# Performance work log

Hardware: AMD Instinct MI355X
Metric: run time of the kernel (lower is better)

The kernel has to match this reference:

```python
import jax, jax.numpy as jnp
import numpy as np


def _bilinear_sample(v, gx, gy, H_, W_):
    # v: (B, H_, W_, nh, Cv); gx, gy: (B, Lq, nh, P) in [0,1] normalized coords.
    # Matches F.grid_sample(mode='bilinear', padding_mode='zeros', align_corners=False).
    x = gx * W_ - 0.5
    y = gy * H_ - 0.5
    x0 = jnp.floor(x)
    y0 = jnp.floor(y)
    dx = x - x0
    dy = y - y0
    x0i = x0.astype(jnp.int32)
    y0i = y0.astype(jnp.int32)
    nh = v.shape[3]
    hidx = jnp.arange(nh)[None, :, None]  # broadcast over (Lq, nh, P)

    def corner(yi, xi):
        valid = (yi >= 0) & (yi < H_) & (xi >= 0) & (xi < W_)
        yc = jnp.clip(yi, 0, H_ - 1)
        xc = jnp.clip(xi, 0, W_ - 1)
        gather = jax.vmap(lambda vb, yb, xb: vb[yb, xb, hidx])  # -> (B, Lq, nh, P, Cv)
        return gather(v, yc, xc) * valid[..., None].astype(v.dtype)

    v00 = corner(y0i, x0i)
    v01 = corner(y0i, x0i + 1)
    v10 = corner(y0i + 1, x0i)
    v11 = corner(y0i + 1, x0i + 1)
    wx0 = (1.0 - dx)[..., None]
    wx1 = dx[..., None]
    wy0 = (1.0 - dy)[..., None]
    wy1 = dy[..., None]
    return wy0 * (wx0 * v00 + wx1 * v01) + wy1 * (wx0 * v10 + wx1 * v11)


def setup_inputs() -> dict:
    key = jax.random.key(0)
    ks = jax.random.split(key, 10)
    C, NH, NL, NP = 256, 8, 4, 4
    B = 1
    shapes = np.array([[128, 128], [64, 64], [32, 32], [16, 16]], dtype=np.int64)
    L_in = int((shapes[:, 0] * shapes[:, 1]).sum())  # 21760
    Lq = L_in
    lsi = np.concatenate([[0], np.cumsum(shapes[:, 0] * shapes[:, 1])[:-1]]).astype(np.int64)

    # sampling_offsets bias init (grid of directions scaled by point index), per _reset_parameters
    thetas = np.arange(NH, dtype=np.float32) * (2.0 * np.pi / NH)
    grid = np.stack([np.cos(thetas), np.sin(thetas)], -1)
    grid = grid / np.abs(grid).max(-1, keepdims=True)
    grid = np.tile(grid[:, None, None, :], (1, NL, NP, 1))
    grid = grid * (np.arange(NP, dtype=np.float32) + 1.0)[None, None, :, None]
    b_off = jnp.asarray(grid.reshape(-1))

    xav = float(np.sqrt(2.0 / (C + C)))
    return {
        "query": jax.random.normal(ks[0], (B, Lq, C), jnp.float32),
        "reference_points": jax.random.uniform(ks[1], (B, Lq, NL, 2), jnp.float32),
        "input_flatten": jax.random.normal(ks[2], (B, L_in, C), jnp.float32),
        "input_spatial_shapes": jnp.asarray(shapes),
        "input_level_start_index": jnp.asarray(lsi),
        "input_padding_mask": jnp.zeros((B, L_in), jnp.bool_),
        "W_off": 0.01 * jax.random.normal(ks[3], (C, NH * NL * NP * 2), jnp.float32),
        "b_off": b_off,
        "W_attn": 0.01 * jax.random.normal(ks[4], (C, NH * NL * NP), jnp.float32),
        "b_attn": jnp.zeros((NH * NL * NP,), jnp.float32),
        "W_v": xav * jax.random.normal(ks[5], (C, C), jnp.float32),
        "b_v": jnp.zeros((C,), jnp.float32),
        "W_out": xav * jax.random.normal(ks[6], (C, C), jnp.float32),
        "b_out": jnp.zeros((C,), jnp.float32),
    }


def reference(query, reference_points, input_flatten, input_spatial_shapes,
              input_level_start_index, input_padding_mask,
              W_off, b_off, W_attn, b_attn, W_v, b_v, W_out, b_out):
    shapes = np.asarray(input_spatial_shapes)  # static spatial shapes (host constants)
    B, Lq, C = query.shape
    NL = shapes.shape[0]
    NH = 8
    Cv = C // NH
    NP = b_off.shape[0] // (NH * NL * 2)

    value = input_flatten @ W_v + b_v
    value = jnp.where(input_padding_mask[..., None], 0.0, value)
    value = value.reshape(B, -1, NH, Cv)

    off = (query @ W_off + b_off).reshape(B, Lq, NH, NL, NP, 2)
    attn = (query @ W_attn + b_attn).reshape(B, Lq, NH, NL * NP)
    attn = jax.nn.softmax(attn, axis=-1).reshape(B, Lq, NH, NL, NP)

    # normalizer is (W, H) per level
    norm = jnp.stack([jnp.asarray(shapes[:, 1]), jnp.asarray(shapes[:, 0])], -1).astype(query.dtype)
    loc = reference_points[:, :, None, :, None, :] + off / norm[None, None, None, :, None, :]

    out = jnp.zeros((B, Lq, NH, Cv), query.dtype)
    start = 0
    for lvl in range(NL):
        H_, W_ = int(shapes[lvl, 0]), int(shapes[lvl, 1])
        v_l = value[:, start:start + H_ * W_].reshape(B, H_, W_, NH, Cv)
        start += H_ * W_
        g = loc[:, :, :, lvl]  # (B, Lq, NH, NP, 2)
        sampled = _bilinear_sample(v_l, g[..., 0], g[..., 1], H_, W_)  # (B, Lq, NH, NP, Cv)
        out = out + jnp.einsum('blhpc,blhp->blhc', sampled, attn[:, :, :, lvl])

    out = out.reshape(B, Lq, C) @ W_out + b_out
    return out  # dropout is identity in eval mode
```

## Files before the change

kernel.cpp:

```cpp
#include <hip/hip_runtime.h>
#include <hip/hip_bf16.h>
#include <hip/hip_fp16.h>


typedef _Float16 f16;
typedef _Float16 f16x8 __attribute__((ext_vector_type(8)));
typedef _Float16 f16x4 __attribute__((ext_vector_type(4)));
typedef _Float16 f16x2 __attribute__((ext_vector_type(2)));
typedef float    f32x4 __attribute__((ext_vector_type(4)));

__device__ __forceinline__ void g2lds16(const void* gp, void* lp) {
    __builtin_amdgcn_global_load_lds(
        (const __attribute__((address_space(1))) unsigned int*)gp,
        (__attribute__((address_space(3))) unsigned int*)lp, 16, 0, 0);
}

template <bool HALF_OUT, bool MASKED>
__global__ __launch_bounds__(512) void gemm_split_f16(
    const f16* __restrict__ A,
    const f16* __restrict__ Bt,
    const float* __restrict__ bias,
    void* __restrict__ Cout, int M, int N,
    const unsigned char* __restrict__ mask)
{
    __shared__ __align__(16) f16 As[64 * 64];
    __shared__ __align__(16) f16 Bs[128 * 64];

    const int tid  = threadIdx.x;
    const int m0   = blockIdx.y * 64, n0 = blockIdx.x * 128;
    const int lane = tid & 63, wid = tid >> 6;
    const int wm   = (wid >> 2) * 32, wn = (wid & 3) * 32;

    f32x4 acc[2][2] = {};

    const int sr  = tid >> 3;
    const int sch = tid & 7;

    for (int kt = 0; kt < 12; ++kt) {
        const int kA = (kt < 8 ? kt : kt - 8) * 64;
        const int kB = kt * 64;
        {
            const int r = sr;
            const int gc = (sch ^ (r & 7)) << 3;
            g2lds16(A + (size_t)(m0 + r) * 512 + kA + gc, &As[r * 64 + sch * 8]);
        }
#pragma unroll
        for (int p = 0; p < 2; ++p) {
            const int r = p * 64 + sr;
            const int gc = (sch ^ (r & 7)) << 3;
            g2lds16(Bt + (size_t)(n0 + r) * 768 + kB + gc, &Bs[r * 64 + sch * 8]);
        }
        __syncthreads();

#pragma unroll
        for (int kf = 0; kf < 2; ++kf) {
            const int kch = kf * 4 + (lane >> 4);
            f16x8 av[2], bv[2];
#pragma unroll
            for (int mf = 0; mf < 2; ++mf) {
                const int row = wm + mf * 16 + (lane & 15);
                av[mf] = *(const f16x8*)&As[row * 64 + ((kch ^ (row & 7)) << 3)];
            }
#pragma unroll
            for (int nf = 0; nf < 2; ++nf) {
                const int row = wn + nf * 16 + (lane & 15);
                bv[nf] = *(const f16x8*)&Bs[row * 64 + ((kch ^ (row & 7)) << 3)];
            }
#pragma unroll
            for (int mf = 0; mf < 2; ++mf)
#pragma unroll
                for (int nf = 0; nf < 2; ++nf)
                    acc[mf][nf] = __builtin_amdgcn_mfma_f32_16x16x32_f16(
                        av[mf], bv[nf], acc[mf][nf], 0, 0, 0);
        }
        __syncthreads();
    }

#pragma unroll
    for (int mf = 0; mf < 2; ++mf) {
        const int rb = m0 + wm + mf * 16 + ((lane >> 4) << 2);
#pragma unroll
        for (int nf = 0; nf < 2; ++nf) {
            const int col = n0 + wn + nf * 16 + (lane & 15);
            const float bc = bias[col];
#pragma unroll
            for (int j = 0; j < 4; ++j) {
                const int row = rb + j;
                float v = acc[mf][nf][j] + bc;
                if (MASKED) v = mask[row] ? 0.f : v;
                if (HALF_OUT)
                    ((__half*)Cout)[(size_t)row * N + col] = __float2half(v);
                else
                    ((float*)Cout)[(size_t)row * N + col] = v;
            }
        }
    }
}

__global__ __launch_bounds__(256) void convA_kernel(
    const float* __restrict__ in, f16* __restrict__ out, int total4)
{
    const int i = blockIdx.x * 256 + threadIdx.x;
    if (i >= total4) return;
    const int m = i >> 6, k4 = (i & 63) << 2;
    const float4 v = reinterpret_cast<const float4*>(in)[i];
    f16x4 hi, lo;
    hi.x = (f16)v.x; lo.x = (f16)(v.x - (float)hi.x);
    hi.y = (f16)v.y; lo.y = (f16)(v.y - (float)hi.y);
    hi.z = (f16)v.z; lo.z = (f16)(v.z - (float)hi.z);
    hi.w = (f16)v.w; lo.w = (f16)(v.w - (float)hi.w);
    *reinterpret_cast<f16x4*>(&out[(size_t)m * 512 + k4])       = hi;
    *reinterpret_cast<f16x4*>(&out[(size_t)m * 512 + 256 + k4]) = lo;
}

__global__ __launch_bounds__(256) void prep_kernel(
    const float* __restrict__ Wv,   const float* __restrict__ Woff,
    const float* __restrict__ Wattn,const float* __restrict__ Wout,
    const float* __restrict__ boff, const float* __restrict__ battn,
    f16* __restrict__ Btv, f16* __restrict__ Btoa, f16* __restrict__ Btout,
    float* __restrict__ boa)
{
    const int i = blockIdx.x * 256 + threadIdx.x;
    constexpr int S0 = 256 * 768, S1 = 256 * 768, S2 = 128 * 768, S3 = 256 * 768;
    if (i < S0) {
        const int n = i / 768, k = i - n * 768, ks = k & 255;
        const float w = Wv[(size_t)ks * 256 + n];
        const f16 h = (f16)w;
        Btv[i] = (k < 512) ? h : (f16)(w - (float)h);
    } else if (i < S0 + S1) {
        const int j = i - S0;
        const int n = j / 768, k = j - n * 768, ks = k & 255;
        const float w = Woff[(size_t)ks * 256 + n];
        const f16 h = (f16)w;
        Btoa[j] = (k < 512) ? h : (f16)(w - (float)h);
    } else if (i < S0 + S1 + S2) {
        const int j = i - S0 - S1;
        const int n = j / 768, k = j - n * 768, ks = k & 255;
        const float w = Wattn[(size_t)ks * 128 + n];
        const f16 h = (f16)w;
        Btoa[(size_t)(256 + n) * 768 + k] = (k < 512) ? h : (f16)(w - (float)h);
    } else if (i < S0 + S1 + S2 + S3) {
        const int j = i - S0 - S1 - S2;
        const int n = j / 768, k = j - n * 768, ks = k & 255;
        const float w = Wout[(size_t)ks * 256 + n];
        const f16 h = (f16)w;
        Btout[j] = (k < 512) ? h : (f16)(w - (float)h);
    } else if (i < S0 + S1 + S2 + S3 + 384) {
        const int j = i - S0 - S1 - S2 - S3;
        boa[j] = (j < 256) ? boff[j] : battn[j - 256];
    }
}

__global__ __launch_bounds__(256) void msda_sample_v2(
    const __half* __restrict__ value,
    const float* __restrict__ offattn,
    const float* __restrict__ refp,
    f16* __restrict__ preA)
{
    __shared__ float s_off[2][256];
    __shared__ float s_ref[2][8];
    __shared__ __align__(16) float s_w[2][512];
    __shared__ __align__(16) int   s_i[2][512];

    const int q0 = blockIdx.x * 2, tid = threadIdx.x;
#pragma unroll
    for (int j = 0; j < 2; ++j) {
        const int idx = tid + j * 256;
        const int ql = idx >> 8, col = idx & 255;
        s_off[ql][col] = offattn[(size_t)(q0 + ql) * 384 + col];
    }
    if (tid < 16) s_ref[tid >> 3][tid & 7] = refp[(size_t)(q0 + (tid >> 3)) * 8 + (tid & 7)];
    __syncthreads();

    {
        const int ql = tid >> 7, slot = tid & 127;
        const int h = slot >> 4, pp = slot & 15, l = pp >> 2, p = pp & 3;
        float v = offattn[(size_t)(q0 + ql) * 384 + 256 + slot];
        float mx = v;
#pragma unroll
        for (int o = 1; o < 16; o <<= 1) mx = fmaxf(mx, __shfl_xor(mx, o, 16));
        const float e = expf(v - mx);
        float s = e;
#pragma unroll
        for (int o = 1; o < 16; o <<= 1) s += __shfl_xor(s, o, 16);
        const float a = e / s;

        const int HW_[4]  = {128, 64, 32, 16};
        const int LSI_[4] = {0, 16384, 20480, 21504};
        const int   Wi = HW_[l];
        const float Wf = (float)Wi;
        const float rx = s_ref[ql][l * 2 + 0], ry = s_ref[ql][l * 2 + 1];
        const float ox = s_off[ql][h * 32 + l * 8 + p * 2 + 0];
        const float oy = s_off[ql][h * 32 + l * 8 + p * 2 + 1];
        const float x = (rx + ox / Wf) * Wf - 0.5f;
        const float y = (ry + oy / Wf) * Wf - 0.5f;
        const float x0f = floorf(x), y0f = floorf(y);
        const float dx = x - x0f, dy = y - y0f;
        const int x0 = (int)x0f, y0 = (int)y0f;
        const int x1 = x0 + 1, y1 = y0 + 1;
        const float vx0 = (x0 >= 0 && x0 < Wi) ? 1.f : 0.f;
        const float vx1 = (x1 >= 0 && x1 < Wi) ? 1.f : 0.f;
        const float vy0 = (y0 >= 0 && y0 < Wi) ? 1.f : 0.f;
        const float vy1 = (y1 >= 0 && y1 < Wi) ? 1.f : 0.f;
        const int xc0 = min(max(x0, 0), Wi - 1), xc1 = min(max(x1, 0), Wi - 1);
        const int yc0 = min(max(y0, 0), Wi - 1), yc1 = min(max(y1, 0), Wi - 1);
        const int base = LSI_[l];
        const int b4 = slot * 4;
        s_i[ql][b4 + 0] = (base + yc0 * Wi + xc0) * 256;
        s_i[ql][b4 + 1] = (base + yc0 * Wi + xc1) * 256;
        s_i[ql][b4 + 2] = (base + yc1 * Wi + xc0) * 256;
        s_i[ql][b4 + 3] = (base + yc1 * Wi + xc1) * 256;
        s_w[ql][b4 + 0] = a * (1.f - dy) * (1.f - dx) * vy0 * vx0;
        s_w[ql][b4 + 1] = a * (1.f - dy) * dx         * vy0 * vx1;
        s_w[ql][b4 + 2] = a * dy         * (1.f - dx) * vy1 * vx0;
        s_w[ql][b4 + 3] = a * dy         * dx         * vy1 * vx1;
    }
    __syncthreads();

    const int ql = tid >> 7, slot = tid & 127;
    const int h = slot >> 4, cp = slot & 15;
    const __half* __restrict__ vb = value + h * 32 + cp * 2;
    float acc0 = 0.f, acc1 = 0.f;
#pragma unroll
    for (int pp = 0; pp < 16; ++pp) {
        const int b = (h * 16 + pp) * 4;
        const int4   idx = *reinterpret_cast<const int4*>(&s_i[ql][b]);
        const float4 w   = *reinterpret_cast<const float4*>(&s_w[ql][b]);
        const __half2 v0 = *reinterpret_cast<const __half2*>(vb + idx.x);
        const __half2 v1 = *reinterpret_cast<const __half2*>(vb + idx.y);
        const __half2 v2 = *reinterpret_cast<const __half2*>(vb + idx.z);
        const __half2 v3 = *reinterpret_cast<const __half2*>(vb + idx.w);
        acc0 = fmaf(w.x, __half2float(v0.x), acc0);
        acc1 = fmaf(w.x, __half2float(v0.y), acc1);
        acc0 = fmaf(w.y, __half2float(v1.x), acc0);
        acc1 = fmaf(w.y, __half2float(v1.y), acc1);
        acc0 = fmaf(w.z, __half2float(v2.x), acc0);
        acc1 = fmaf(w.z, __half2float(v2.y), acc1);
        acc0 = fmaf(w.w, __half2float(v3.x), acc0);
        acc1 = fmaf(w.w, __half2float(v3.y), acc1);
    }
    const int q = q0 + ql;
    const f16 h0 = (f16)acc0, h1 = (f16)acc1;
    const f16 l0 = (f16)(acc0 - (float)h0), l1 = (f16)(acc1 - (float)h1);
    f16x2 hv; hv.x = h0; hv.y = h1;
    f16x2 lv; lv.x = l0; lv.y = l1;
    *reinterpret_cast<f16x2*>(&preA[(size_t)q * 512 + h * 32 + cp * 2])       = hv;
    *reinterpret_cast<f16x2*>(&preA[(size_t)q * 512 + 256 + h * 32 + cp * 2]) = lv;
}

extern "C" void kernel_launch(void* const* d_in, const int* in_sizes, int n_in,
                              void* d_out, int out_size, void* d_ws, size_t ws_size,
                              hipStream_t stream)
{
    const float*         query  = (const float*)d_in[0];
    const float*         refp   = (const float*)d_in[1];
    const float*         inF    = (const float*)d_in[2];
    const unsigned char* mask   = (const unsigned char*)d_in[5];
    const float*         W_off  = (const float*)d_in[6];
    const float*         b_off  = (const float*)d_in[7];
    const float*         W_attn = (const float*)d_in[8];
    const float*         b_attn = (const float*)d_in[9];
    const float*         W_v    = (const float*)d_in[10];
    const float*         b_v    = (const float*)d_in[11];
    const float*         W_out  = (const float*)d_in[12];
    const float*         b_out  = (const float*)d_in[13];
    float*               out    = (float*)d_out;

    const int M = in_sizes[0] / 256;
    if (M % 128 != 0) return;

    const size_t SZ_A1  = (size_t)M * 512 * sizeof(f16);
    const size_t SZ_VAL = (size_t)M * 256 * sizeof(__half);
    const size_t SZ_OA  = (size_t)M * 384 * sizeof(float);
    const size_t SZ_BTV = 256 * 768 * sizeof(f16);
    const size_t SZ_BTO = 384 * 768 * sizeof(f16);
    char* w = (char*)d_ws;
    f16*    A1     = (f16*)w;                      w += SZ_A1;
    __half* valueH = (__half*)w;                   w += SZ_VAL;
    float*  offattn= (float*)w;                    w += SZ_OA;
    f16*    Btv    = (f16*)w;                      w += SZ_BTV;
    f16*    Btoa   = (f16*)w;                      w += SZ_BTO;
    f16*    Btout  = (f16*)w;                      w += SZ_BTV;
    float*  boa    = (float*)w;                    w += 512 * sizeof(float);
    if ((size_t)(w - (char*)d_ws) > ws_size) return;

    const dim3 blk256(256), blk512(512);
    const int convA_blocks = (M * 64 + 255) / 256;
    const int prep_total = 3 * 256 * 768 + 128 * 768 + 384;

    prep_kernel<<<dim3((prep_total + 255) / 256), blk256, 0, stream>>>(
        W_v, W_off, W_attn, W_out, b_off, b_attn, Btv, Btoa, Btout, boa);

    convA_kernel<<<dim3(convA_blocks), blk256, 0, stream>>>(inF, A1, M * 64);
    gemm_split_f16<true, true><<<dim3(2, M / 64), blk512, 0, stream>>>(
        A1, Btv, b_v, valueH, M, 256, mask);

    convA_kernel<<<dim3(convA_blocks), blk256, 0, stream>>>(query, A1, M * 64);
    gemm_split_f16<false, false><<<dim3(3, M / 64), blk512, 0, stream>>>(
        A1, Btoa, boa, offattn, M, 384, nullptr);

    msda_sample_v2<<<dim3(M / 2), blk256, 0, stream>>>(valueH, offattn, refp, A1);

    gemm_split_f16<false, false><<<dim3(2, M / 64), blk512, 0, stream>>>(
        A1, Btout, b_out, out, M, 256, nullptr);
}
```

Measured before the change: 229.2 us.

## Fuse fp32-to-split-f16 conversion into GEMM and double-buffer LDS tiles

Removes the separate convA kernels. Each GEMM now loads its fp32 A rows into registers once and converts them in-kernel into hi/lo f16 parts. The GEMM LDS tiles are double-buffered so the next B tile is fetched and the next A tile staged while MFMAs run on the current one, which drops one barrier per k-step. The sampling kernel writes fp32 output directly (no split) and pads its shared index/weight arrays to reduce bank conflicts. This cuts two kernel launches and the A1 intermediate round-trip through memory, at the cost of more registers and LDS per GEMM block.

```diff
diff --git a/kernel.cpp b/kernel.cpp
--- a/kernel.cpp
+++ b/kernel.cpp
@@ -5,8 +5,6 @@
 
 typedef _Float16 f16;
 typedef _Float16 f16x8 __attribute__((ext_vector_type(8)));
-typedef _Float16 f16x4 __attribute__((ext_vector_type(4)));
-typedef _Float16 f16x2 __attribute__((ext_vector_type(2)));
 typedef float    f32x4 __attribute__((ext_vector_type(4)));
 
 __device__ __forceinline__ void g2lds16(const void* gp, void* lp) {
@@ -16,64 +14,94 @@
 }
 
 template <bool HALF_OUT, bool MASKED>
-__global__ __launch_bounds__(512) void gemm_split_f16(
-    const f16* __restrict__ A,
+__global__ __launch_bounds__(512) void gemm_f32a(
+    const float* __restrict__ Af,
     const f16* __restrict__ Bt,
     const float* __restrict__ bias,
     void* __restrict__ Cout, int M, int N,
     const unsigned char* __restrict__ mask)
 {
-    __shared__ __align__(16) f16 As[64 * 64];
-    __shared__ __align__(16) f16 Bs[128 * 64];
+    __shared__ __align__(16) f16 As[2][64 * 64];
+    __shared__ __align__(16) f16 Bs[2][128 * 64];
 
     const int tid  = threadIdx.x;
     const int m0   = blockIdx.y * 64, n0 = blockIdx.x * 128;
     const int lane = tid & 63, wid = tid >> 6;
     const int wm   = (wid >> 2) * 32, wn = (wid & 3) * 32;
 
+    const int arow = tid >> 3;
+    const int acb  = tid & 7;
+    float4 ar[4][2];
+#pragma unroll
+    for (int g = 0; g < 4; ++g)
+#pragma unroll
+        for (int h2 = 0; h2 < 2; ++h2)
+            ar[g][h2] = *reinterpret_cast<const float4*>(
+                Af + (size_t)(m0 + arow) * 256 + g * 64 + acb * 8 + h2 * 4);
+
     f32x4 acc[2][2] = {};
 
+    auto stageA = [&](int buf, int kt) {
+        const int  g  = kt < 4 ? kt : (kt < 8 ? kt - 4 : kt - 8);
+        const bool lo = (kt >= 4 && kt < 8);
+        f16x8 v;
+#pragma unroll
+        for (int h2 = 0; h2 < 2; ++h2) {
+            const float4 f = ar[g][h2];
+            const float fv[4] = {f.x, f.y, f.z, f.w};
+#pragma unroll
+            for (int j = 0; j < 4; ++j) {
+                const f16 hi = (f16)fv[j];
+                v[h2 * 4 + j] = lo ? (f16)(fv[j] - (float)hi) : hi;
+            }
+        }
+        const int cc = acb ^ (arow & 7);
+        *reinterpret_cast<f16x8*>(&As[buf][arow * 64 + cc * 8]) = v;
+    };
     const int sr  = tid >> 3;
     const int sch = tid & 7;
-
+    auto stageB = [&](int buf, int kt) {
+#pragma unroll
+        for (int p = 0; p < 2; ++p) {
+            const int r  = p * 64 + sr;
+            const int gc = (sch ^ (r & 7)) << 3;
+            g2lds16(Bt + (size_t)(n0 + r) * 768 + kt * 64 + gc,
+                    &Bs[buf][r * 64 + sch * 8]);
+        }
+    };
+
+    stageB(0, 0);
+    stageA(0, 0);
+
+#pragma unroll
     for (int kt = 0; kt < 12; ++kt) {
-        const int kA = (kt < 8 ? kt : kt - 8) * 64;
-        const int kB = kt * 64;
-        {
-            const int r = sr;
-            const int gc = (sch ^ (r & 7)) << 3;
-            g2lds16(A + (size_t)(m0 + r) * 512 + kA + gc, &As[r * 64 + sch * 8]);
-        }
-#pragma unroll
-        for (int p = 0; p < 2; ++p) {
-            const int r = p * 64 + sr;
-            const int gc = (sch ^ (r & 7)) << 3;
-            g2lds16(Bt + (size_t)(n0 + r) * 768 + kB + gc, &Bs[r * 64 + sch * 8]);
-        }
+        const int cur = kt & 1;
         __syncthreads();
 
+        f16x8 av[2][2], bv[2][2];
 #pragma unroll
         for (int kf = 0; kf < 2; ++kf) {
             const int kch = kf * 4 + (lane >> 4);
-            f16x8 av[2], bv[2];
 #pragma unroll
             for (int mf = 0; mf < 2; ++mf) {
                 const int row = wm + mf * 16 + (lane & 15);
-                av[mf] = *(const f16x8*)&As[row * 64 + ((kch ^ (row & 7)) << 3)];
+                av[kf][mf] = *(const f16x8*)&As[cur][row * 64 + ((kch ^ (row & 7)) << 3)];
             }
 #pragma unroll
             for (int nf = 0; nf < 2; ++nf) {
                 const int row = wn + nf * 16 + (lane & 15);
-                bv[nf] = *(const f16x8*)&Bs[row * 64 + ((kch ^ (row & 7)) << 3)];
+                bv[kf][nf] = *(const f16x8*)&Bs[cur][row * 64 + ((kch ^ (row & 7)) << 3)];
             }
+        }
+        if (kt < 11) { stageB(cur ^ 1, kt + 1); stageA(cur ^ 1, kt + 1); }
+#pragma unroll
+        for (int kf = 0; kf < 2; ++kf)
 #pragma unroll
             for (int mf = 0; mf < 2; ++mf)
 #pragma unroll
                 for (int nf = 0; nf < 2; ++nf)
                     acc[mf][nf] = __builtin_amdgcn_mfma_f32_16x16x32_f16(
-                        av[mf], bv[nf], acc[mf][nf], 0, 0, 0);
-        }
-        __syncthreads();
+                        av[kf][mf], bv[kf][nf], acc[mf][nf], 0, 0, 0);
     }
 
 #pragma unroll
@@ -95,22 +123,6 @@
             }
         }
     }
-}
-
-__global__ __launch_bounds__(256) void convA_kernel(
-    const float* __restrict__ in, f16* __restrict__ out, int total4)
-{
-    const int i = blockIdx.x * 256 + threadIdx.x;
-    if (i >= total4) return;
-    const int m = i >> 6, k4 = (i & 63) << 2;
-    const float4 v = reinterpret_cast<const float4*>(in)[i];
-    f16x4 hi, lo;
-    hi.x = (f16)v.x; lo.x = (f16)(v.x - (float)hi.x);
-    hi.y = (f16)v.y; lo.y = (f16)(v.y - (float)hi.y);
-    hi.z = (f16)v.z; lo.z = (f16)(v.z - (float)hi.z);
-    hi.w = (f16)v.w; lo.w = (f16)(v.w - (float)hi.w);
-    *reinterpret_cast<f16x4*>(&out[(size_t)m * 512 + k4])       = hi;
-    *reinterpret_cast<f16x4*>(&out[(size_t)m * 512 + 256 + k4]) = lo;
 }
 
 __global__ __launch_bounds__(256) void prep_kernel(
@@ -151,16 +163,16 @@
     }
 }
 
-__global__ __launch_bounds__(256) void msda_sample_v2(
+__global__ __launch_bounds__(256) void msda_sample_v3(
     const __half* __restrict__ value,
     const float* __restrict__ offattn,
     const float* __restrict__ refp,
-    f16* __restrict__ preA)
+    float* __restrict__ pre)
 {
     __shared__ float s_off[2][256];
     __shared__ float s_ref[2][8];
-    __shared__ __align__(16) float s_w[2][512];
-    __shared__ __align__(16) int   s_i[2][512];
+    __shared__ __align__(16) float s_w[2][576];
+    __shared__ __align__(16) int   s_i[2][576];
 
     const int q0 = blockIdx.x * 2, tid = threadIdx.x;
 #pragma unroll
@@ -205,31 +217,32 @@
         const int xc0 = min(max(x0, 0), Wi - 1), xc1 = min(max(x1, 0), Wi - 1);
         const int yc0 = min(max(y0, 0), Wi - 1), yc1 = min(max(y1, 0), Wi - 1);
         const int base = LSI_[l];
-        const int b4 = slot * 4;
-        s_i[ql][b4 + 0] = (base + yc0 * Wi + xc0) * 256;
-        s_i[ql][b4 + 1] = (base + yc0 * Wi + xc1) * 256;
-        s_i[ql][b4 + 2] = (base + yc1 * Wi + xc0) * 256;
-        s_i[ql][b4 + 3] = (base + yc1 * Wi + xc1) * 256;
-        s_w[ql][b4 + 0] = a * (1.f - dy) * (1.f - dx) * vy0 * vx0;
-        s_w[ql][b4 + 1] = a * (1.f - dy) * dx         * vy0 * vx1;
-        s_w[ql][b4 + 2] = a * dy         * (1.f - dx) * vy1 * vx0;
-        s_w[ql][b4 + 3] = a * dy         * dx         * vy1 * vx1;
+        const int eI = h * 72 + pp * 4;
+        s_i[ql][eI + 0] = (base + yc0 * Wi + xc0) * 512;
+        s_i[ql][eI + 1] = (base + yc0 * Wi + xc1) * 512;
+        s_i[ql][eI + 2] = (base + yc1 * Wi + xc0) * 512;
+        s_i[ql][eI + 3] = (base + yc1 * Wi + xc1) * 512;
+        s_w[ql][eI + 0] = a * (1.f - dy) * (1.f - dx) * vy0 * vx0;
+        s_w[ql][eI + 1] = a * (1.f - dy) * dx         * vy0 * vx1;
+        s_w[ql][eI + 2] = a * dy         * (1.f - dx) * vy1 * vx0;
+        s_w[ql][eI + 3] = a * dy         * dx         * vy1 * vx1;
     }
     __syncthreads();
 
     const int ql = tid >> 7, slot = tid & 127;
     const int h = slot >> 4, cp = slot & 15;
-    const __half* __restrict__ vb = value + h * 32 + cp * 2;
+    const int lb = h * 64 + cp * 4;
+    const char* __restrict__ vbase = (const char*)value;
     float acc0 = 0.f, acc1 = 0.f;
 #pragma unroll
     for (int pp = 0; pp < 16; ++pp) {
-        const int b = (h * 16 + pp) * 4;
-        const int4   idx = *reinterpret_cast<const int4*>(&s_i[ql][b]);
-        const float4 w   = *reinterpret_cast<const float4*>(&s_w[ql][b]);
-        const __half2 v0 = *reinterpret_cast<const __half2*>(vb + idx.x);
-        const __half2 v1 = *reinterpret_cast<const __half2*>(vb + idx.y);
-        const __half2 v2 = *reinterpret_cast<const __half2*>(vb + idx.z);
-        const __half2 v3 = *reinterpret_cast<const __half2*>(vb + idx.w);
+        const int eI = h * 72 + pp * 4;
+        const int4   idx = *reinterpret_cast<const int4*>(&s_i[ql][eI]);
+        const float4 w   = *reinterpret_cast<const float4*>(&s_w[ql][eI]);
+        const __half2 v0 = *reinterpret_cast<const __half2*>(vbase + (idx.x + lb));
+        const __half2 v1 = *reinterpret_cast<const __half2*>(vbase + (idx.y + lb));
+        const __half2 v2 = *reinterpret_cast<const __half2*>(vbase + (idx.z + lb));
+        const __half2 v3 = *reinterpret_cast<const __half2*>(vbase + (idx.w + lb));
         acc0 = fmaf(w.x, __half2float(v0.x), acc0);
         acc1 = fmaf(w.x, __half2float(v0.y), acc1);
         acc0 = fmaf(w.y, __half2float(v1.x), acc0);
@@ -239,13 +252,8 @@
         acc0 = fmaf(w.w, __half2float(v3.x), acc0);
         acc1 = fmaf(w.w, __half2float(v3.y), acc1);
     }
-    const int q = q0 + ql;
-    const f16 h0 = (f16)acc0, h1 = (f16)acc1;
-    const f16 l0 = (f16)(acc0 - (float)h0), l1 = (f16)(acc1 - (float)h1);
-    f16x2 hv; hv.x = h0; hv.y = h1;
-    f16x2 lv; lv.x = l0; lv.y = l1;
-    *reinterpret_cast<f16x2*>(&preA[(size_t)q * 512 + h * 32 + cp * 2])       = hv;
-    *reinterpret_cast<f16x2*>(&preA[(size_t)q * 512 + 256 + h * 32 + cp * 2]) = lv;
+    float2 o; o.x = acc0; o.y = acc1;
+    *reinterpret_cast<float2*>(&pre[(size_t)(q0 + ql) * 256 + h * 32 + cp * 2]) = o;
 }
 
 extern "C" void kernel_launch(void* const* d_in, const int* in_sizes, int n_in,
@@ -269,15 +277,15 @@
     const int M = in_sizes[0] / 256;
     if (M % 128 != 0) return;
 
-    const size_t SZ_A1  = (size_t)M * 512 * sizeof(f16);
     const size_t SZ_VAL = (size_t)M * 256 * sizeof(__half);
     const size_t SZ_OA  = (size_t)M * 384 * sizeof(float);
+    const size_t SZ_PRE = (size_t)M * 256 * sizeof(float);
     const size_t SZ_BTV = 256 * 768 * sizeof(f16);
     const size_t SZ_BTO = 384 * 768 * sizeof(f16);
     char* w = (char*)d_ws;
-    f16*    A1     = (f16*)w;                      w += SZ_A1;
     __half* valueH = (__half*)w;                   w += SZ_VAL;
     float*  offattn= (float*)w;                    w += SZ_OA;
+    float*  pre    = (float*)w;                    w += SZ_PRE;
     f16*    Btv    = (f16*)w;                      w += SZ_BTV;
     f16*    Btoa   = (f16*)w;                      w += SZ_BTO;
     f16*    Btout  = (f16*)w;                      w += SZ_BTV;
@@ -285,22 +293,19 @@
     if ((size_t)(w - (char*)d_ws) > ws_size) return;
 
     const dim3 blk256(256), blk512(512);
-    const int convA_blocks = (M * 64 + 255) / 256;
     const int prep_total = 3 * 256 * 768 + 128 * 768 + 384;
 
     prep_kernel<<<dim3((prep_total + 255) / 256), blk256, 0, stream>>>(
         W_v, W_off, W_attn, W_out, b_off, b_attn, Btv, Btoa, Btout, boa);
 
-    convA_kernel<<<dim3(convA_blocks), blk256, 0, stream>>>(inF, A1, M * 64);
-    gemm_split_f16<true, true><<<dim3(2, M / 64), blk512, 0, stream>>>(
-        A1, Btv, b_v, valueH, M, 256, mask);
-
-    convA_kernel<<<dim3(convA_blocks), blk256, 0, stream>>>(query, A1, M * 64);
-    gemm_split_f16<false, false><<<dim3(3, M / 64), blk512, 0, stream>>>(
-        A1, Btoa, boa, offattn, M, 384, nullptr);
-
-    msda_sample_v2<<<dim3(M / 2), blk256, 0, stream>>>(valueH, offattn, refp, A1);
-
-    gemm_split_f16<false, false><<<dim3(2, M / 64), blk512, 0, stream>>>(
-        A1, Btout, b_out, out, M, 256, nullptr);
-}
+    gemm_f32a<true, true><<<dim3(2, M / 64), blk512, 0, stream>>>(
+        inF, Btv, b_v, valueH, M, 256, mask);
+
+    gemm_f32a<false, false><<<dim3(3, M / 64), blk512, 0, stream>>>(
+        query, Btoa, boa, offattn, M, 384, nullptr);
+
+    msda_sample_v3<<<dim3(M / 2), blk256, 0, stream>>>(valueH, offattn, refp, pre);
+
+    gemm_f32a<false, false><<<dim3(2, M / 64), blk512, 0, stream>>>(
+        pre, Btout, b_out, out, M, 256, nullptr);
+}
```

Measured after the change: 225.6 us. No clear change (-1.6%).
